# Optimization experiments

Hardware: AMD Instinct MI355X
Metric: run time of the kernel (lower is better)

Reference implementation:

```python
import jax, jax.numpy as jnp
import numpy as np

ITER = 6
GAMMA = 0.99
Q = 0.95


def _maxpool(x, win, stride, pad):
    # NCHW max pool
    return jax.lax.reduce_window(
        x, -jnp.inf, jax.lax.max,
        (1, 1, win, win), (1, 1, stride, stride),
        ((0, 0), (0, 0), (pad, pad), (pad, pad)))


def _nearest(x, size):
    # torch F.interpolate(mode='nearest'): src = floor(dst * in / out)
    H, W = size
    h_in, w_in = x.shape[2], x.shape[3]
    ih = (jnp.arange(H) * h_in) // H
    iw = (jnp.arange(W) * w_in) // W
    return x[:, :, ih[:, None], iw[None, :]]


def setup_inputs() -> dict:
    key = jax.random.key(0)
    ks = jax.random.split(key, 4)
    C, mid = 256, 16  # mid = int(sqrt(C))
    x = jax.random.normal(ks[0], (16, C, 128, 128), jnp.float32)
    w1 = jax.random.normal(ks[1], (mid, C), jnp.float32) / np.sqrt(C)
    b1 = jnp.zeros((mid,), jnp.float32)
    w2 = jax.random.normal(ks[2], (C, mid), jnp.float32) / np.sqrt(mid)
    b2 = jnp.zeros((C,), jnp.float32)
    return {"x": x, "w1": w1, "b1": b1, "w2": w2, "b2": b2}


def reference(x, w1, b1, w2, b2):
    B, C, H, W = x.shape
    # --- quantile activation mask (detached) ---
    flat = x.reshape(B, C, H * W)
    thr = jnp.quantile(flat, Q, axis=-1)[:, :, None, None]  # [B,C,1,1]
    M = jax.lax.stop_gradient((x >= thr).astype(x.dtype))
    # --- propagate field ---
    feat = x * M
    out = feat
    for i in range(ITER):
        g = jnp.asarray(GAMMA ** (2 ** i), x.dtype)
        if i == 0:
            feat = _maxpool(feat, 3, 1, 1) * g  # same-resolution 3x3 pool
            out = jnp.maximum(out, feat)
        else:
            # 5x5 stride-2 pool -> scale -> nearest upsample back to (H,W)
            feat = _nearest(_maxpool(feat, 5, 2, 2) * g, (H, W))
            out = jnp.maximum(out, feat)
    # --- receptor modulator: 1x1 conv -> relu -> 1x1 conv -> sigmoid ---
    h = jax.nn.relu(jnp.einsum('bchw,mc->bmhw', out, w1) + b1[None, :, None, None])
    R = jax.nn.sigmoid(jnp.einsum('bmhw,cm->bchw', h, w2) + b2[None, :, None, None])
    y = x * R
    return y
```

## Files before the change

kernel.cpp:

```cpp
#include <hip/hip_runtime.h>
#include <cmath>
#include <cfloat>

#define HW_ 16384

__device__ __forceinline__ unsigned f2key(float f){
    unsigned u = __float_as_uint(f);
    return u ^ ((u & 0x80000000u) ? 0xFFFFFFFFu : 0x80000000u);
}
__device__ __forceinline__ float key2f(unsigned k){
    unsigned u = (k & 0x80000000u) ? (k ^ 0x80000000u) : ~k;
    return __uint_as_float(u);
}
__device__ __forceinline__ unsigned short f2bf(float f){
    unsigned u = __float_as_uint(f);
    unsigned r = u + 0x7FFFu + ((u >> 16) & 1u);
    return (unsigned short)(r >> 16);
}
__device__ __forceinline__ float bf2f(unsigned short s){
    return __uint_as_float((unsigned)s << 16);
}
__device__ __forceinline__ unsigned pkmax(unsigned a, unsigned b){
    unsigned d;
    asm("v_pk_max_u16 %0, %1, %2" : "=v"(d) : "v"(a), "v"(b));
    return d;
}
__device__ __forceinline__ unsigned alignb(unsigned hi, unsigned lo){
    unsigned d;
    asm("v_alignbit_b32 %0, %1, %2, 16" : "=v"(d) : "v"(hi), "v"(lo));
    return d;
}
__device__ __forceinline__ unsigned cvtpk(float lo, float hi){
    unsigned d;
    asm("v_cvt_pk_bf16_f32 %0, %1, %2" : "=v"(d) : "v"(lo), "v"(hi));
    return d;
}
__device__ __forceinline__ unsigned wscan_incl(unsigned v, int lane){
    #pragma unroll
    for (int o = 1; o < 64; o <<= 1){
        unsigned u = __shfl_up(v, o);
        v += (lane >= o) ? u : 0u;
    }
    return v;
}

typedef short bf16x8 __attribute__((ext_vector_type(8)));
typedef float f32x4  __attribute__((ext_vector_type(4)));
__device__ __forceinline__ bf16x8 tofrag(uint4 q){
    union { uint4 q; bf16x8 f; } u; u.q = q; return u.f;
}

__global__ __launch_bounds__(512, 6) void k1f(
    const float* __restrict__ x,
    unsigned short* __restrict__ outp, unsigned short* __restrict__ m64g,
    float g1, float q2, float q3, float q4, float q5, float q6)
{
    __shared__ __align__(16) unsigned short C0[16384];
    __shared__ __align__(16) unsigned short H5s[8192];
    __shared__ unsigned hist[1024];
    __shared__ unsigned wsum[8];
    __shared__ unsigned redA[8], redB[8];
    __shared__ unsigned s_dA, s_dB, s_cloA, s_cloB, s_keyA, s_keyB;

    const int tid = threadIdx.x;
    const int lane = tid & 63;
    const int wid = tid >> 6;
    const unsigned bc = blockIdx.x;
    const float4* xp4 = (const float4*)(x + (size_t)bc * HW_);

    unsigned key[32];

    #pragma unroll
    for (int k = 0; k < 2; ++k) hist[tid + k * 512] = 0u;
    __syncthreads();
    #pragma unroll
    for (int k = 0; k < 8; ++k){
        float4 v = xp4[tid + k * 512];
        key[4*k+0] = f2key(v.x);
        key[4*k+1] = f2key(v.y);
        key[4*k+2] = f2key(v.z);
        key[4*k+3] = f2key(v.w);
        atomicAdd(&hist[key[4*k+0] >> 22], 1u);
        atomicAdd(&hist[key[4*k+1] >> 22], 1u);
        atomicAdd(&hist[key[4*k+2] >> 22], 1u);
        atomicAdd(&hist[key[4*k+3] >> 22], 1u);
    }
    __syncthreads();

    unsigned rA = 15563u, rB = 15564u;
    unsigned prefVal = 0u, prefMask = 0u;
    bool done = false;

    {
        unsigned part = hist[tid*2] + hist[tid*2+1];
        unsigned incl = wscan_incl(part, lane);
        if (lane == 63) wsum[wid] = incl;
        __syncthreads();
        unsigned off = 0;
        #pragma unroll
        for (int w = 0; w < 8; ++w) off += (w < wid) ? wsum[w] : 0u;
        unsigned phi = incl + off;
        unsigned plo = phi - part;
        if (rA >= plo && rA < phi){
            unsigned c = plo;
            #pragma unroll
            for (int k = 0; k < 2; ++k){
                unsigned hh = hist[tid*2+k];
                if (rA < c + hh){ s_dA = tid*2+k; s_cloA = c; break; }
                c += hh;
            }
        }
        if (rB >= plo && rB < phi){
            unsigned c = plo;
            #pragma unroll
            for (int k = 0; k < 2; ++k){
                unsigned hh = hist[tid*2+k];
                if (rB < c + hh){ s_dB = tid*2+k; s_cloB = c; break; }
                c += hh;
            }
        }
        __syncthreads();
        unsigned dA = s_dA, dB = s_dB;
        if (dA != dB){
            unsigned locA = 0u, locB = 0xFFFFFFFFu;
            #pragma unroll
            for (int e = 0; e < 32; ++e){
                unsigned d = key[e] >> 22;
                if (d == dA) locA = max(locA, key[e]);
                if (d == dB) locB = min(locB, key[e]);
            }
            #pragma unroll
            for (int o = 32; o > 0; o >>= 1){
                locA = max(locA, __shfl_down(locA, o));
                locB = min(locB, __shfl_down(locB, o));
            }
            if (lane == 0){ redA[wid] = locA; redB[wid] = locB; }
            __syncthreads();
            if (tid == 0){
                unsigned a = redA[0], b = redB[0];
                for (int w = 1; w < 8; ++w){ a = max(a, redA[w]); b = min(b, redB[w]); }
                s_keyA = a; s_keyB = b;
            }
            __syncthreads();
            done = true;
        } else {
            prefVal = dA << 22; prefMask = 0x3FFu << 22;
            rA -= s_cloA; rB -= s_cloB;
            __syncthreads();
        }
    }

    if (!done){
        const int shifts[3] = {14, 6, 0};
        const int bitsv[3]  = {8, 8, 6};
        for (int lvl = 0; lvl < 3 && !done; ++lvl){
            int shift = shifts[lvl];
            unsigned nb = 1u << bitsv[lvl];
            unsigned msk = nb - 1u;
            if (tid < (int)nb) hist[tid] = 0u;
            __syncthreads();
            #pragma unroll
            for (int e = 0; e < 32; ++e){
                if ((key[e] & prefMask) == prefVal)
                    atomicAdd(&hist[(key[e] >> shift) & msk], 1u);
            }
            __syncthreads();
            unsigned part = (tid < (int)nb) ? hist[tid] : 0u;
            unsigned incl = wscan_incl(part, lane);
            if (lane == 63) wsum[wid] = incl;
            __syncthreads();
            unsigned off = 0;
            #pragma unroll
            for (int w = 0; w < 8; ++w) off += (w < wid) ? wsum[w] : 0u;
            unsigned phi = incl + off;
            unsigned plo = phi - part;
            if (tid < (int)nb){
                if (rA >= plo && rA < phi){ s_dA = tid; s_cloA = plo; }
                if (rB >= plo && rB < phi){ s_dB = tid; s_cloB = plo; }
            }
            __syncthreads();
            unsigned dA = s_dA, dB = s_dB;
            if (dA != dB){
                unsigned mA = prefMask | (msk << shift);
                unsigned vAp = prefVal | (dA << shift);
                unsigned vBp = prefVal | (dB << shift);
                unsigned locA = 0u, locB = 0xFFFFFFFFu;
                #pragma unroll
                for (int e = 0; e < 32; ++e){
                    if ((key[e] & mA) == vAp) locA = max(locA, key[e]);
                    if ((key[e] & mA) == vBp) locB = min(locB, key[e]);
                }
                #pragma unroll
                for (int o = 32; o > 0; o >>= 1){
                    locA = max(locA, __shfl_down(locA, o));
                    locB = min(locB, __shfl_down(locB, o));
                }
                if (lane == 0){ redA[wid] = locA; redB[wid] = locB; }
                __syncthreads();
                if (tid == 0){
                    unsigned a = redA[0], b = redB[0];
                    for (int w = 1; w < 8; ++w){ a = max(a, redA[w]); b = min(b, redB[w]); }
                    s_keyA = a; s_keyB = b;
                }
                __syncthreads();
                done = true;
            } else {
                prefVal |= dA << shift;
                prefMask |= msk << shift;
                rA -= s_cloA; rB -= s_cloB;
                if (lvl == 2){
                    if (tid == 0){ s_keyA = prefVal; s_keyB = prefVal; }
                    done = true;
                }
                __syncthreads();
            }
        }
    }

    float vlo = key2f(s_keyA);
    float vhi = key2f(s_keyB);
    float idxq = 0.95f * 16383.0f;
    float frac = idxq - floorf(idxq);
    const float thr = vlo * (1.0f - frac) + vhi * frac;

    #pragma unroll
    for (int k = 0; k < 8; ++k){
        int i = tid + k * 512;
        float f0 = key2f(key[4*k+0]); f0 = (f0 >= thr) ? f0 : 0.0f;
        float f1 = key2f(key[4*k+1]); f1 = (f1 >= thr) ? f1 : 0.0f;
        float f2 = key2f(key[4*k+2]); f2 = (f2 >= thr) ? f2 : 0.0f;
        float f3 = key2f(key[4*k+3]); f3 = (f3 >= thr) ? f3 : 0.0f;
        uint2 w; w.x = cvtpk(f0, f1); w.y = cvtpk(f2, f3);
        ((uint2*)C0)[i] = w;
    }
    __syncthreads();

    {
        const unsigned* C0w = (const unsigned*)C0;
        unsigned* outp32 = (unsigned*)(outp + (size_t)bc * HW_);
        const int wc = lane;
        const int r0 = wid * 16;

        unsigned hmA, hmB, hmC, cB, cC;
        {
            int r = r0 - 1;
            if (r < 0){ hmA = 0u; }
            else {
                unsigned w = C0w[r*64 + wc];
                unsigned wl = __shfl_up(w, 1);
                unsigned wr = __shfl_down(w, 1);
                if (wc == 0)  wl = 0u;
                if (wc == 63) wr = 0u;
                hmA = pkmax(pkmax(alignb(w, wl), w), alignb(wr, w));
            }
        }
        {
            int r = r0;
            unsigned w = C0w[r*64 + wc];
            unsigned wl = __shfl_up(w, 1);
            unsigned wr = __shfl_down(w, 1);
            if (wc == 0)  wl = 0u;
            if (wc == 63) wr = 0u;
            hmB = pkmax(pkmax(alignb(w, wl), w), alignb(wr, w));
            cB = w;
        }
        #pragma unroll
        for (int rr = 0; rr < 16; ++rr){
            int r = r0 + rr;
            {
                int rn = r + 1;
                if (rn > 127){ hmC = 0u; cC = 0u; }
                else {
                    unsigned w = C0w[rn*64 + wc];
                    unsigned wl = __shfl_up(w, 1);
                    unsigned wr = __shfl_down(w, 1);
                    if (wc == 0)  wl = 0u;
                    if (wc == 63) wr = 0u;
                    hmC = pkmax(pkmax(alignb(w, wl), w), alignb(wr, w));
                    cC = w;
                }
            }
            unsigned p1 = pkmax(pkmax(hmA, hmB), hmC);
            float a0 = g1 * bf2f((unsigned short)(p1 & 0xFFFFu));
            float a1v = g1 * bf2f((unsigned short)(p1 >> 16));
            outp32[r*64 + wc] = pkmax(cB, cvtpk(a0, a1v));
            unsigned wjm1 = __shfl_up(p1, 1);
            unsigned wjp1 = __shfl_down(p1, 1);
            if (wc == 0)  wjm1 = 0u;
            if (wc == 63) wjp1 = 0u;
            unsigned s = pkmax(wjm1, p1);
            s = pkmax(s, s >> 16);
            s = pkmax(s, wjp1 & 0xFFFFu);
            H5s[r*64 + wc] = (unsigned short)s;
            hmA = hmB; hmB = hmC; cB = cC;
        }
    }
    __syncthreads();

    unsigned* U = (unsigned*)C0;
    unsigned* T = ((unsigned*)C0) + 2048;
    float mf[8];
    #pragma unroll
    for (int k = 0; k < 4; ++k){
        int q = tid + k * 512;
        int i = q >> 5, wj = q & 31;
        int rr = 2 * i;
        const unsigned* H5w = (const unsigned*)H5s;
        unsigned m = pkmax(H5w[rr*32 + wj], H5w[(rr+1)*32 + wj]);
        if (rr >= 1) m = pkmax(m, H5w[(rr-1)*32 + wj]);
        if (rr >= 2) m = pkmax(m, H5w[(rr-2)*32 + wj]);
        if (rr + 2 <= 127) m = pkmax(m, H5w[(rr+2)*32 + wj]);
        U[q] = m;
        mf[2*k]   = q2 * bf2f((unsigned short)(m & 0xFFFFu));
        mf[2*k+1] = q2 * bf2f((unsigned short)(m >> 16));
    }
    __syncthreads();

    const float gs[4] = {q3, q4, q5, q6};
    #pragma unroll
    for (int it = 0; it < 4; ++it){
        #pragma unroll
        for (int k = 0; k < 4; ++k){
            int q = tid + k * 512;
            unsigned w = U[q];
            unsigned wl = __shfl_up(w, 1);
            unsigned wr = __shfl_down(w, 1);
            if ((q & 31) == 0)  wl = 0u;
            if ((q & 31) == 31) wr = 0u;
            T[q] = pkmax(pkmax(alignb(w, wl), w), alignb(wr, w));
        }
        __syncthreads();
        #pragma unroll
        for (int k = 0; k < 4; ++k){
            int q = tid + k * 512;
            int r = q >> 5;
            unsigned w = T[q];
            if (r > 0)  w = pkmax(w, T[q - 32]);
            if (r < 63) w = pkmax(w, T[q + 32]);
            U[q] = w;
            mf[2*k]   = fmaxf(mf[2*k],   gs[it] * bf2f((unsigned short)(w & 0xFFFFu)));
            mf[2*k+1] = fmaxf(mf[2*k+1], gs[it] * bf2f((unsigned short)(w >> 16)));
        }
        __syncthreads();
    }

    {
        unsigned* mp = (unsigned*)(m64g + (size_t)bc * 4096);
        #pragma unroll
        for (int k = 0; k < 4; ++k){
            int q = tid + k * 512;
            mp[q] = cvtpk(mf[2*k], mf[2*k+1]);
        }
    }
}

__global__ __launch_bounds__(256) void k3_mfma(
    const float* __restrict__ x, const unsigned short* __restrict__ outp,
    const unsigned short* __restrict__ m64,
    const float* __restrict__ w1, const float* __restrict__ b1,
    const float* __restrict__ w2, const float* __restrict__ b2,
    float* __restrict__ y)
{
    __shared__ __align__(16) unsigned short SOUT[16384];
    __shared__ __align__(16) unsigned short W1h[16*264];
    __shared__ __align__(16) unsigned short W1l[16*264];
    __shared__ __align__(16) unsigned short W2s[256*40];
    __shared__ __align__(16) float HS[4*16*18];

    const int tid  = threadIdx.x;
    const int lane = tid & 63;
    const int wid  = tid >> 6;
    const int blk  = blockIdx.x;
    const int b    = blk >> 8;
    const int px0  = (blk & 255) * 64;

    for (int e = tid; e < 4096; e += 256){
        int m = e >> 8, c = e & 255;
        float f = w1[m*256 + c];
        unsigned short hi = f2bf(f);
        W1h[m*264 + c] = hi;
        W1l[m*264 + c] = f2bf(f - bf2f(hi));
    }
    for (int e = tid; e < 4096; e += 256){
        int c = e >> 4, m = e & 15;
        float f = w2[e];
        unsigned short hi = f2bf(f);
        W2s[c*40 + m]      = hi;
        W2s[c*40 + 16 + m] = f2bf(f - bf2f(hi));
    }
    {
        const int row = px0 >> 7;
        const int mibase = (row >> 1)*64 + ((px0 & 127) >> 1);
        const unsigned* op32 = (const unsigned*)(outp + (size_t)b*256*HW_);
        const unsigned short* mp = m64 + (size_t)b*256*4096;
        #pragma unroll
        for (int i = 0; i < 32; ++i){
            int u = tid + i*256;
            int ch = u >> 5, pxp = u & 31;
            unsigned o2 = op32[(ch*HW_ + px0)/2 + pxp];
            unsigned short mv = mp[ch*4096 + mibase + pxp];
            unsigned v = pkmax(o2, (unsigned)mv * 0x10001u);
            int pa = 2*pxp, pb = pa + 1;
            SOUT[(pa*512 + ((ch*2) ^ ((pa & 30) << 3))) >> 1] = (unsigned short)v;
            SOUT[(pb*512 + ((ch*2) ^ ((pb & 30) << 3))) >> 1] = (unsigned short)(v >> 16);
        }
    }
    __syncthreads();

    const int nidx = lane & 15;
    const int kg   = lane >> 4;
    const int px_t = wid*16 + nidx;

    f32x4 acc = {0.f, 0.f, 0.f, 0.f};
    #pragma unroll
    for (int ks = 0; ks < 8; ++ks){
        int byteB = px_t*512 + ((ks*64 + kg*16) ^ ((px_t & 30) << 3));
        uint4 qb = *(const uint4*)((const char*)SOUT + byteB);
        bf16x8 fb = tofrag(qb);
        int byteA = nidx*528 + ks*64 + kg*16;
        uint4 qh = *(const uint4*)((const char*)W1h + byteA);
        uint4 ql = *(const uint4*)((const char*)W1l + byteA);
        acc = __builtin_amdgcn_mfma_f32_16x16x32_bf16(tofrag(qh), fb, acc, 0, 0, 0);
        acc = __builtin_amdgcn_mfma_f32_16x16x32_bf16(tofrag(ql), fb, acc, 0, 0, 0);
    }
    #pragma unroll
    for (int i2 = 0; i2 < 4; ++i2){
        int mid = kg*4 + i2;
        float hv = fmaxf(acc[i2] + b1[mid], 0.0f);
        HS[(wid*16 + nidx)*18 + mid] = hv;
    }
    __syncthreads();

    bf16x8 bh = {0,0,0,0,0,0,0,0}, bl = {0,0,0,0,0,0,0,0};
    if (kg < 2){
        const float* hp = &HS[(wid*16 + nidx)*18 + kg*8];
        float f0 = hp[0], f1 = hp[1], f2 = hp[2], f3 = hp[3];
        float f4 = hp[4], f5 = hp[5], f6 = hp[6], f7 = hp[7];
        unsigned short h0 = f2bf(f0), h1 = f2bf(f1), h2 = f2bf(f2), h3 = f2bf(f3);
        unsigned short h4 = f2bf(f4), h5 = f2bf(f5), h6 = f2bf(f6), h7 = f2bf(f7);
        bh[0] = (short)h0; bh[1] = (short)h1; bh[2] = (short)h2; bh[3] = (short)h3;
        bh[4] = (short)h4; bh[5] = (short)h5; bh[6] = (short)h6; bh[7] = (short)h7;
        bl[0] = (short)f2bf(f0 - bf2f(h0)); bl[1] = (short)f2bf(f1 - bf2f(h1));
        bl[2] = (short)f2bf(f2 - bf2f(h2)); bl[3] = (short)f2bf(f3 - bf2f(h3));
        bl[4] = (short)f2bf(f4 - bf2f(h4)); bl[5] = (short)f2bf(f5 - bf2f(h5));
        bl[6] = (short)f2bf(f6 - bf2f(h6)); bl[7] = (short)f2bf(f7 - bf2f(h7));
    }

    #pragma unroll 4
    for (int t = 0; t < 16; ++t){
        bf16x8 a2h = {0,0,0,0,0,0,0,0}, a2l = {0,0,0,0,0,0,0,0};
        if (kg < 2){
            const char* basep = (const char*)W2s + (t*16 + nidx)*80;
            a2h = tofrag(*(const uint4*)(basep + kg*16));
            a2l = tofrag(*(const uint4*)(basep + 32 + kg*16));
        }
        f32x4 d2 = {0.f, 0.f, 0.f, 0.f};
        d2 = __builtin_amdgcn_mfma_f32_16x16x32_bf16(a2h, bh, d2, 0, 0, 0);
        d2 = __builtin_amdgcn_mfma_f32_16x16x32_bf16(a2l, bh, d2, 0, 0, 0);
        d2 = __builtin_amdgcn_mfma_f32_16x16x32_bf16(a2h, bl, d2, 0, 0, 0);
        #pragma unroll
        for (int i2 = 0; i2 < 4; ++i2){
            int ch = t*16 + kg*4 + i2;
            float logit = d2[i2] + b2[ch];
            float R = 1.0f / (1.0f + __expf(-logit));
            size_t gidx = ((size_t)(b*256 + ch))*HW_ + px0 + px_t;
            y[gidx] = x[gidx] * R;
        }
    }
}

extern "C" void kernel_launch(void* const* d_in, const int* in_sizes, int n_in,
                              void* d_out, int out_size, void* d_ws, size_t ws_size,
                              hipStream_t stream) {
    const float* x  = (const float*)d_in[0];
    const float* w1 = (const float*)d_in[1];
    const float* b1 = (const float*)d_in[2];
    const float* w2 = (const float*)d_in[3];
    const float* b2 = (const float*)d_in[4];
    float* y  = (float*)d_out;
    char* ws = (char*)d_ws;

    unsigned short* outp = (unsigned short*)ws;
    unsigned short* m64  = (unsigned short*)(ws + 134217728);

    float g1 = 0.99f;
    float q2 = (float)std::pow(0.99, 3.0);
    float q3 = (float)std::pow(0.99, 7.0);
    float q4 = (float)std::pow(0.99, 15.0);
    float q5 = (float)std::pow(0.99, 31.0);
    float q6 = (float)std::pow(0.99, 63.0);

    k1f<<<4096, 512, 0, stream>>>(x, outp, m64, g1, q2, q3, q4, q5, q6);
    k3_mfma<<<4096, 256, 0, stream>>>(x, outp, m64, w1, b1, w2, b2, y);
}
```

Baseline: 349.3 us.

## Precompute bf16 weight splits once and read them from global memory in k3

```diff
diff --git a/kernel.cpp b/kernel.cpp
--- a/kernel.cpp
+++ b/kernel.cpp
@@ -48,6 +48,26 @@
 typedef float f32x4  __attribute__((ext_vector_type(4)));
 __device__ __forceinline__ bf16x8 tofrag(uint4 q){
     union { uint4 q; bf16x8 f; } u; u.q = q; return u.f;
+}
+
+__global__ __launch_bounds__(256) void k0_split(
+    const float* __restrict__ w1, const float* __restrict__ w2,
+    unsigned short* __restrict__ W1h, unsigned short* __restrict__ W1l,
+    unsigned short* __restrict__ W2h, unsigned short* __restrict__ W2l)
+{
+    int e = blockIdx.x * 256 + threadIdx.x;
+    if (e < 4096){
+        float f = w1[e];
+        unsigned short hi = f2bf(f);
+        W1h[e] = hi;
+        W1l[e] = f2bf(f - bf2f(hi));
+    } else {
+        int e2 = e - 4096;
+        float f = w2[e2];
+        unsigned short hi = f2bf(f);
+        W2h[e2] = hi;
+        W2l[e2] = f2bf(f - bf2f(hi));
+    }
 }
 
 __global__ __launch_bounds__(512, 6) void k1f(
@@ -355,16 +375,14 @@
 }
 
 __global__ __launch_bounds__(256) void k3_mfma(
-    const float* __restrict__ x, const unsigned short* __restrict__ outp,
-    const unsigned short* __restrict__ m64,
-    const float* __restrict__ w1, const float* __restrict__ b1,
-    const float* __restrict__ w2, const float* __restrict__ b2,
+    const float* __restrict__ x,
+    const unsigned short* __restrict__ outp, const unsigned short* __restrict__ m64,
+    const unsigned short* __restrict__ W1h, const unsigned short* __restrict__ W1l,
+    const unsigned short* __restrict__ W2h, const unsigned short* __restrict__ W2l,
+    const float* __restrict__ b1, const float* __restrict__ b2,
     float* __restrict__ y)
 {
-    __shared__ __align__(16) unsigned short SOUT[16384];
-    __shared__ __align__(16) unsigned short W1h[16*264];
-    __shared__ __align__(16) unsigned short W1l[16*264];
-    __shared__ __align__(16) unsigned short W2s[256*40];
+    __shared__ __align__(16) unsigned SOUT32[8192];
     __shared__ __align__(16) float HS[4*16*18];
 
     const int tid  = threadIdx.x;
@@ -374,35 +392,27 @@
     const int b    = blk >> 8;
     const int px0  = (blk & 255) * 64;
 
-    for (int e = tid; e < 4096; e += 256){
-        int m = e >> 8, c = e & 255;
-        float f = w1[m*256 + c];
-        unsigned short hi = f2bf(f);
-        W1h[m*264 + c] = hi;
-        W1l[m*264 + c] = f2bf(f - bf2f(hi));
-    }
-    for (int e = tid; e < 4096; e += 256){
-        int c = e >> 4, m = e & 15;
-        float f = w2[e];
-        unsigned short hi = f2bf(f);
-        W2s[c*40 + m]      = hi;
-        W2s[c*40 + 16 + m] = f2bf(f - bf2f(hi));
-    }
     {
         const int row = px0 >> 7;
         const int mibase = (row >> 1)*64 + ((px0 & 127) >> 1);
         const unsigned* op32 = (const unsigned*)(outp + (size_t)b*256*HW_);
         const unsigned short* mp = m64 + (size_t)b*256*4096;
         #pragma unroll
-        for (int i = 0; i < 32; ++i){
-            int u = tid + i*256;
-            int ch = u >> 5, pxp = u & 31;
-            unsigned o2 = op32[(ch*HW_ + px0)/2 + pxp];
-            unsigned short mv = mp[ch*4096 + mibase + pxp];
-            unsigned v = pkmax(o2, (unsigned)mv * 0x10001u);
-            int pa = 2*pxp, pb = pa + 1;
-            SOUT[(pa*512 + ((ch*2) ^ ((pa & 30) << 3))) >> 1] = (unsigned short)v;
-            SOUT[(pb*512 + ((ch*2) ^ ((pb & 30) << 3))) >> 1] = (unsigned short)(v >> 16);
+        for (int i = 0; i < 16; ++i){
+            int u = i*256 + tid;
+            int c4 = u >> 5, pxp = u & 31;
+            int ch0 = 2*c4;
+            unsigned wA = op32[ch0*(HW_/2) + px0/2 + pxp];
+            unsigned wB = op32[(ch0+1)*(HW_/2) + px0/2 + pxp];
+            unsigned mA = (unsigned)mp[ch0*4096 + mibase + pxp] * 0x10001u;
+            unsigned mB = (unsigned)mp[(ch0+1)*4096 + mibase + pxp] * 0x10001u;
+            unsigned va = pkmax(wA, mA);
+            unsigned vb = pkmax(wB, mB);
+            unsigned wpa = (va & 0xFFFFu) | (vb << 16);
+            unsigned wpb = (va >> 16) | (vb & 0xFFFF0000u);
+            int sw = (pxp & 7) << 2;
+            SOUT32[(2*pxp)  *128 + (c4 ^ sw)] = wpa;
+            SOUT32[(2*pxp+1)*128 + (c4 ^ sw)] = wpb;
         }
     }
     __syncthreads();
@@ -410,18 +420,17 @@
     const int nidx = lane & 15;
     const int kg   = lane >> 4;
     const int px_t = wid*16 + nidx;
+    const int sxz  = ((px_t >> 1) & 7) << 2;
 
     f32x4 acc = {0.f, 0.f, 0.f, 0.f};
     #pragma unroll
     for (int ks = 0; ks < 8; ++ks){
-        int byteB = px_t*512 + ((ks*64 + kg*16) ^ ((px_t & 30) << 3));
-        uint4 qb = *(const uint4*)((const char*)SOUT + byteB);
-        bf16x8 fb = tofrag(qb);
-        int byteA = nidx*528 + ks*64 + kg*16;
-        uint4 qh = *(const uint4*)((const char*)W1h + byteA);
-        uint4 ql = *(const uint4*)((const char*)W1l + byteA);
-        acc = __builtin_amdgcn_mfma_f32_16x16x32_bf16(tofrag(qh), fb, acc, 0, 0, 0);
-        acc = __builtin_amdgcn_mfma_f32_16x16x32_bf16(tofrag(ql), fb, acc, 0, 0, 0);
+        int w0 = (ks*16 + kg*4) ^ sxz;
+        bf16x8 fb = tofrag(*(const uint4*)&SOUT32[px_t*128 + w0]);
+        bf16x8 ah = tofrag(*(const uint4*)(W1h + nidx*256 + ks*32 + kg*8));
+        bf16x8 al = tofrag(*(const uint4*)(W1l + nidx*256 + ks*32 + kg*8));
+        acc = __builtin_amdgcn_mfma_f32_16x16x32_bf16(ah, fb, acc, 0, 0, 0);
+        acc = __builtin_amdgcn_mfma_f32_16x16x32_bf16(al, fb, acc, 0, 0, 0);
     }
     #pragma unroll
     for (int i2 = 0; i2 < 4; ++i2){
@@ -450,9 +459,8 @@
     for (int t = 0; t < 16; ++t){
         bf16x8 a2h = {0,0,0,0,0,0,0,0}, a2l = {0,0,0,0,0,0,0,0};
         if (kg < 2){
-            const char* basep = (const char*)W2s + (t*16 + nidx)*80;
-            a2h = tofrag(*(const uint4*)(basep + kg*16));
-            a2l = tofrag(*(const uint4*)(basep + 32 + kg*16));
+            a2h = tofrag(*(const uint4*)(W2h + (t*16 + nidx)*16 + kg*8));
+            a2l = tofrag(*(const uint4*)(W2l + (t*16 + nidx)*16 + kg*8));
         }
         f32x4 d2 = {0.f, 0.f, 0.f, 0.f};
         d2 = __builtin_amdgcn_mfma_f32_16x16x32_bf16(a2h, bh, d2, 0, 0, 0);
@@ -482,6 +490,10 @@
 
     unsigned short* outp = (unsigned short*)ws;
     unsigned short* m64  = (unsigned short*)(ws + 134217728);
+    unsigned short* W1h  = (unsigned short*)(ws + 167772160);
+    unsigned short* W1l  = W1h + 4096;
+    unsigned short* W2h  = W1h + 8192;
+    unsigned short* W2l  = W1h + 12288;
 
     float g1 = 0.99f;
     float q2 = (float)std::pow(0.99, 3.0);
@@ -490,6 +502,7 @@
     float q5 = (float)std::pow(0.99, 31.0);
     float q6 = (float)std::pow(0.99, 63.0);
 
+    k0_split<<<32, 256, 0, stream>>>(w1, w2, W1h, W1l, W2h, W2l);
     k1f<<<4096, 512, 0, stream>>>(x, outp, m64, g1, q2, q3, q4, q5, q6);
-    k3_mfma<<<4096, 256, 0, stream>>>(x, outp, m64, w1, b1, w2, b2, y);
-}
+    k3_mfma<<<4096, 256, 0, stream>>>(x, outp, m64, W1h, W1l, W2h, W2l, b1, b2, y);
+}
```

New measurement: 336.4 us. 3.7% less time.
